# Kernel tuning notes

Hardware: AMD Instinct MI355X
Metric: run time of the kernel (lower is better)

Reference implementation:

```python
import jax, jax.numpy as jnp
import numpy as np

B, P, C, D, H = 32, 2048, 19, 512, 4
DH = D // H  # 128
EPS = 1e-5


def setup_inputs() -> dict:
    key = jax.random.key(0)
    ks = jax.random.split(key, 12)
    s = 0.02
    return {
        "x": jax.random.normal(ks[0], (B, P, D), jnp.float32),
        "channel_embeddings": jax.random.normal(ks[1], (C, D), jnp.float32),
        "Wq": jax.random.normal(ks[2], (D, D), jnp.float32) * s,
        "bq": jnp.zeros((D,), jnp.float32),
        "Wk": jax.random.normal(ks[3], (D, D), jnp.float32) * s,
        "bk": jnp.zeros((D,), jnp.float32),
        "Wv": jax.random.normal(ks[4], (D, D), jnp.float32) * s,
        "bv": jnp.zeros((D,), jnp.float32),
        "Wo": jax.random.normal(ks[5], (D, D), jnp.float32) * s,
        "bo": jnp.zeros((D,), jnp.float32),
        "gamma": jnp.ones((D,), jnp.float32),
        "beta": jnp.zeros((D,), jnp.float32),
    }


def reference(x, channel_embeddings, Wq, bq, Wk, bk, Wv, bv, Wo, bo, gamma, beta):
    # q: (B, P, H, DH)
    q = (x @ Wq.T + bq).reshape(B, P, H, DH)
    # K/V depend only on channel embeddings (same for every batch/patch in the
    # original; it merely materialized the broadcast). Compute once: (C, H, DH)
    k = (channel_embeddings @ Wk.T + bk).reshape(C, H, DH)
    v = (channel_embeddings @ Wv.T + bv).reshape(C, H, DH)
    # scores over channels: (B, P, C, H)
    scores = jnp.einsum("bphd,chd->bpch", q, k) / jnp.sqrt(jnp.float32(DH))
    weights = jax.nn.softmax(scores, axis=2)  # softmax over channel dim
    # weighted sum of channel values: (B, P, H, DH) -> (B, P, D)
    attended = jnp.einsum("bpch,chd->bphd", weights, v).reshape(B, P, D)
    out = attended @ Wo.T + bo  # dropout is identity in eval mode
    # residual + layernorm
    h = x + out
    mean = jnp.mean(h, axis=-1, keepdims=True)
    var = jnp.mean(jnp.square(h - mean), axis=-1, keepdims=True)
    return (h - mean) * jax.lax.rsqrt(var + EPS) * gamma + beta
```

## Files before the change

### kernel.cpp

```cpp
#include <hip/hip_runtime.h>
#include <hip/hip_bf16.h>

#define C_  19
#define D_  512
#define H_  4
#define DH_ 128
#define NROW 65536
#define CHP_ 96

typedef float f32x4 __attribute__((ext_vector_type(4)));
typedef short bf16x8 __attribute__((ext_vector_type(8)));

__device__ __forceinline__ unsigned short f2bf(float f) {
  union { __hip_bfloat16 h; unsigned short s; } u;
  u.h = __float2bfloat16(f);
  return u.s;
}
__device__ __forceinline__ float bf2f(unsigned short h) {
  return __uint_as_float(((unsigned int)h) << 16);
}
__device__ __forceinline__ bf16x8 ld_cvt8(const float* p) {
  f32x4 v0 = *(const f32x4*)p;
  f32x4 v1 = *(const f32x4*)(p + 4);
  bf16x8 a;
  a[0]=(short)f2bf(v0[0]); a[1]=(short)f2bf(v0[1]);
  a[2]=(short)f2bf(v0[2]); a[3]=(short)f2bf(v0[3]);
  a[4]=(short)f2bf(v1[0]); a[5]=(short)f2bf(v1[1]);
  a[6]=(short)f2bf(v1[2]); a[7]=(short)f2bf(v1[3]);
  return a;
}
__device__ __forceinline__ float dot4(f32x4 a, f32x4 b, float acc) {
  return fmaf(a[0],b[0], fmaf(a[1],b[1], fmaf(a[2],b[2], fmaf(a[3],b[3], acc))));
}

__global__ __launch_bounds__(512) void prep(
    const float* __restrict__ ce,
    const float* __restrict__ Wq, const float* __restrict__ bq,
    const float* __restrict__ Wk, const float* __restrict__ bk,
    const float* __restrict__ Wv, const float* __restrict__ bv,
    const float* __restrict__ Wo, const float* __restrict__ bo,
    unsigned short* __restrict__ Mtf, unsigned short* __restrict__ Utf,
    float* __restrict__ s0g)
{
  __shared__ __attribute__((aligned(16))) float KV[2][DH_];
  __shared__ float KVp[512];

  const int p = blockIdx.x;
  const int m = threadIdx.x;
  const int mt_off = (p>>4)*8192 + (m>>5)*512 + ((((m>>3)&3)<<4) + (p&15))*8 + (m&7);
  const int ut_off = ((m>>4)*3 + (p>>5))*512 + ((((p>>3)&3)<<4) + (m&15))*8 + (p&7);
  const int c = p >> 2, h = p & 3;

  if (c >= C_) {
    if (p < 80) { Mtf[mt_off] = 0; if (m == 0) s0g[p] = 0.f; }
    Utf[ut_off] = (p == 80) ? f2bf(bo[m]) : (unsigned short)0;
    return;
  }

  {
    const int which = m >> 8;
    const int dh    = (m >> 1) & 127;
    const int half  = m & 1;
    const float* w = (which ? Wv : Wk) + (size_t)(h*DH_ + dh)*D_ + half*256;
    const float* e = ce + (size_t)c*D_ + half*256;
    float a0 = 0.f, a1 = 0.f, a2 = 0.f, a3 = 0.f;
    #pragma unroll
    for (int d = 0; d < 256; d += 16) {
      a0 = dot4(*(const f32x4*)(w+d   ), *(const f32x4*)(e+d   ), a0);
      a1 = dot4(*(const f32x4*)(w+d+4 ), *(const f32x4*)(e+d+4 ), a1);
      a2 = dot4(*(const f32x4*)(w+d+8 ), *(const f32x4*)(e+d+8 ), a2);
      a3 = dot4(*(const f32x4*)(w+d+12), *(const f32x4*)(e+d+12), a3);
    }
    KVp[m] = (a0 + a1) + (a2 + a3);
  }
  __syncthreads();
  if (m < 256) {
    const int which = m >> 7, dh = m & 127;
    KV[which][dh] = KVp[2*m] + KVp[2*m+1] + (which ? bv : bk)[h*DH_ + dh];
  }
  __syncthreads();

  const float rs128 = 0.08838834764831843f;

  {
    float m0 = 0.f, m1 = 0.f, m2 = 0.f, m3 = 0.f;
    const float* wq = Wq + (size_t)(h*DH_)*D_ + m;
    #pragma unroll 8
    for (int dh = 0; dh < DH_; dh += 4) {
      m0 = fmaf(wq[(size_t)(dh  )*D_], KV[0][dh  ], m0);
      m1 = fmaf(wq[(size_t)(dh+1)*D_], KV[0][dh+1], m1);
      m2 = fmaf(wq[(size_t)(dh+2)*D_], KV[0][dh+2], m2);
      m3 = fmaf(wq[(size_t)(dh+3)*D_], KV[0][dh+3], m3);
    }
    Mtf[mt_off] = f2bf(((m0 + m1) + (m2 + m3)) * rs128);
  }

  {
    const float* wor = Wo + (size_t)m*D_ + h*DH_;
    float u0 = 0.f, u1 = 0.f, u2 = 0.f, u3 = 0.f;
    #pragma unroll
    for (int dh = 0; dh < DH_; dh += 16) {
      u0 = dot4(*(const f32x4*)(wor+dh   ), *(const f32x4*)(&KV[1][dh   ]), u0);
      u1 = dot4(*(const f32x4*)(wor+dh+4 ), *(const f32x4*)(&KV[1][dh+4 ]), u1);
      u2 = dot4(*(const f32x4*)(wor+dh+8 ), *(const f32x4*)(&KV[1][dh+8 ]), u2);
      u3 = dot4(*(const f32x4*)(wor+dh+12), *(const f32x4*)(&KV[1][dh+12]), u3);
    }
    Utf[ut_off] = f2bf((u0 + u1) + (u2 + u3));
  }

  if (m == 0) {
    float sa = 0.f;
    for (int dh = 0; dh < DH_; ++dh) sa = fmaf(bq[h*DH_+dh], KV[0][dh], sa);
    s0g[p] = sa * rs128;
  }
}

__global__ __launch_bounds__(256) void fused64(
    const float* __restrict__ x,
    const unsigned short* __restrict__ Mtf,
    const unsigned short* __restrict__ Utf,
    const float* __restrict__ s0g,
    const float* __restrict__ gamma, const float* __restrict__ beta,
    float* __restrict__ out)
{
  __shared__ __attribute__((aligned(16))) unsigned short Xbf[64*512];
  __shared__ __attribute__((aligned(16))) unsigned short WaL[64][104];
  __shared__ float rs_[64][2], rq_[64][2];

  const int t    = threadIdx.x;
  const int wave = t >> 6;
  const int lane = t & 63;
  const int lhi  = lane >> 4;
  const int llo  = lane & 15;
  const int row0 = blockIdx.x * 64;
  const int wrow = wave * 16;

  {
    #pragma unroll
    for (int j = 0; j < 16; ++j) {
      bf16x8 a = ld_cvt8(x + (size_t)(row0 + wrow + j)*D_ + lane*8);
      int byteoff = (wrow + j)*1024 + ((lane*16) ^ ((j & 7) << 4));
      *(bf16x8*)((char*)Xbf + byteoff) = a;
    }
  }
  asm volatile("s_waitcnt lgkmcnt(0)" ::: "memory");
  __builtin_amdgcn_sched_barrier(0);

  {
    const char* xb = (const char*)Xbf + (wrow + llo)*1024;
    const int swz = (llo & 7) << 4;
    f32x4 acc0 = (f32x4){0,0,0,0}, acc1 = acc0, acc2 = acc0, acc3 = acc0, acc4 = acc0;
    #pragma unroll
    for (int ks = 0; ks < 16; ++ks) {
      bf16x8 a = *(const bf16x8*)(xb + ((ks*64 + lhi*16) ^ swz));
      acc0 = __builtin_amdgcn_mfma_f32_16x16x32_bf16(a, *(const bf16x8*)(Mtf + 0*8192 + ks*512 + lane*8), acc0, 0, 0, 0);
      acc1 = __builtin_amdgcn_mfma_f32_16x16x32_bf16(a, *(const bf16x8*)(Mtf + 1*8192 + ks*512 + lane*8), acc1, 0, 0, 0);
      acc2 = __builtin_amdgcn_mfma_f32_16x16x32_bf16(a, *(const bf16x8*)(Mtf + 2*8192 + ks*512 + lane*8), acc2, 0, 0, 0);
      acc3 = __builtin_amdgcn_mfma_f32_16x16x32_bf16(a, *(const bf16x8*)(Mtf + 3*8192 + ks*512 + lane*8), acc3, 0, 0, 0);
      acc4 = __builtin_amdgcn_mfma_f32_16x16x32_bf16(a, *(const bf16x8*)(Mtf + 4*8192 + ks*512 + lane*8), acc4, 0, 0, 0);
    }
    const bool dead = (llo >= 12);
    float s0v0 = s0g[llo], s0v1 = s0g[16+llo], s0v2 = s0g[32+llo],
          s0v3 = s0g[48+llo], s0v4 = s0g[64+llo];
    #pragma unroll
    for (int r = 0; r < 4; ++r) {
      float v0 = acc0[r] + s0v0;
      float v1 = acc1[r] + s0v1;
      float v2 = acc2[r] + s0v2;
      float v3 = acc3[r] + s0v3;
      float v4 = dead ? -1e30f : (acc4[r] + s0v4);
      float mx = fmaxf(fmaxf(fmaxf(v0, v1), fmaxf(v2, v3)), v4);
      mx = fmaxf(mx, __shfl_xor(mx, 4, 64));
      mx = fmaxf(mx, __shfl_xor(mx, 8, 64));
      float e0 = __expf(v0 - mx), e1 = __expf(v1 - mx), e2 = __expf(v2 - mx),
            e3 = __expf(v3 - mx), e4 = dead ? 0.f : __expf(v4 - mx);
      float sm = e0 + e1 + e2 + e3 + e4;
      sm += __shfl_xor(sm, 4, 64);
      sm += __shfl_xor(sm, 8, 64);
      float inv = 1.f / sm;
      int lr = wrow + lhi*4 + r;
      WaL[lr][     llo] = f2bf(e0 * inv);
      WaL[lr][16 + llo] = f2bf(e1 * inv);
      WaL[lr][32 + llo] = f2bf(e2 * inv);
      WaL[lr][48 + llo] = f2bf(e3 * inv);
      WaL[lr][64 + llo] = f2bf(e4 * inv);
    }
    {
      int prow = wrow + lhi*4 + (llo & 3);
      int cj   = llo >> 2;
      WaL[prow][80 + cj*4 + 0] = (cj == 0) ? (unsigned short)0x3F80 : (unsigned short)0;
      WaL[prow][80 + cj*4 + 1] = 0;
      WaL[prow][80 + cj*4 + 2] = 0;
      WaL[prow][80 + cj*4 + 3] = 0;
    }
  }
  __syncthreads();

  const int rg = wave >> 1;
  const int cs = wave & 1;
  #pragma unroll
  for (int ha = 0; ha < 2; ++ha) {
    const int hrow = ha * 32;
    f32x4 oacc[16];
    #pragma unroll
    for (int i = 0; i < 16; ++i) oacc[i] = (f32x4){0.f,0.f,0.f,0.f};
    #pragma unroll
    for (int ks = 0; ks < 3; ++ks) {
      bf16x8 a = *(const bf16x8*)&WaL[hrow + rg*16 + llo][ks*32 + lhi*8];
      #pragma unroll
      for (int tile = 0; tile < 16; ++tile) {
        int ntile = cs*16 + tile;
        bf16x8 b = *(const bf16x8*)(Utf + (size_t)(ntile*3 + ks)*512 + lane*8);
        oacc[tile] = __builtin_amdgcn_mfma_f32_16x16x32_bf16(a, b, oacc[tile], 0, 0, 0);
      }
    }

    float s[4] = {0,0,0,0}, q[4] = {0,0,0,0};
    #pragma unroll
    for (int tile = 0; tile < 16; ++tile) {
      int n = cs*256 + tile*16 + llo;
      #pragma unroll
      for (int r = 0; r < 4; ++r) {
        int m = hrow + rg*16 + lhi*4 + r;
        float xres = bf2f(*(const unsigned short*)
            ((const char*)Xbf + m*1024 + ((n*2) ^ ((m & 7) << 4))));
        float val = oacc[tile][r] + xres;
        oacc[tile][r] = val;
        s[r] += val;
        q[r] = fmaf(val, val, q[r]);
      }
    }
    #pragma unroll
    for (int r = 0; r < 4; ++r) {
      #pragma unroll
      for (int off = 1; off < 16; off <<= 1) {
        s[r] += __shfl_xor(s[r], off, 64);
        q[r] += __shfl_xor(q[r], off, 64);
      }
    }
    if (llo == 0) {
      #pragma unroll
      for (int r = 0; r < 4; ++r) {
        rs_[hrow + rg*16 + lhi*4 + r][cs] = s[r];
        rq_[hrow + rg*16 + lhi*4 + r][cs] = q[r];
      }
    }
    __syncthreads();
    float mu_r[4], rstd_r[4];
    #pragma unroll
    for (int r = 0; r < 4; ++r) {
      int m = hrow + rg*16 + lhi*4 + r;
      float sum = rs_[m][0] + rs_[m][1];
      float sq  = rq_[m][0] + rq_[m][1];
      float mu  = sum * (1.f/(float)D_);
      float var = sq * (1.f/(float)D_) - mu*mu;
      mu_r[r]   = mu;
      rstd_r[r] = rsqrtf(var + 1e-5f);
    }
    #pragma unroll
    for (int tile = 0; tile < 16; ++tile) {
      int n = cs*256 + tile*16 + llo;
      float g = gamma[n], bt = beta[n];
      #pragma unroll
      for (int r = 0; r < 4; ++r) {
        int m = hrow + rg*16 + lhi*4 + r;
        out[(size_t)(row0 + m)*D_ + n] = (oacc[tile][r] - mu_r[r]) * rstd_r[r] * g + bt;
      }
    }
  }
}

extern "C" void kernel_launch(void* const* d_in, const int* in_sizes, int n_in,
                              void* d_out, int out_size, void* d_ws, size_t ws_size,
                              hipStream_t stream) {
  const float* x     = (const float*)d_in[0];
  const float* ce    = (const float*)d_in[1];
  const float* Wq    = (const float*)d_in[2];
  const float* bq    = (const float*)d_in[3];
  const float* Wk    = (const float*)d_in[4];
  const float* bk    = (const float*)d_in[5];
  const float* Wv    = (const float*)d_in[6];
  const float* bv    = (const float*)d_in[7];
  const float* Wo    = (const float*)d_in[8];
  const float* bo    = (const float*)d_in[9];
  const float* gamma = (const float*)d_in[10];
  const float* beta  = (const float*)d_in[11];
  float* out = (float*)d_out;

  char* ws = (char*)d_ws;
  unsigned short* Mtf = (unsigned short*)(ws);
  unsigned short* Utf = (unsigned short*)(ws + 81920);
  float* s0g          = (float*)(ws + 180224);

  prep<<<CHP_, 512, 0, stream>>>(ce, Wq, bq, Wk, bk, Wv, bv, Wo, bo,
                                 Mtf, Utf, s0g);
  fused64<<<NROW/64, 256, 0, stream>>>(x, Mtf, Utf, s0g, gamma, beta, out);
}
```

Before: 123.0 us.

## Split each 64-row tile across eight waves instead of four

The fused kernel now launches 512 threads per 64-row block, so each wave handles 8 rows in the first GEMM and a single 16-row half of the output GEMM and LayerNorm, instead of looping over two halves. The goal is more waves in flight per block and a shorter serial chain per wave, which helps latency hiding. In exchange, half of each first-stage MFMA's rows are redundant: lanes duplicate rows via llo&7 and only lhi<2 write. Launch bounds of 512 with a minimum of 4 blocks per unit also constrain register use.

After: 123.9 us. Within noise of the previous version (+0.7%).

```diff
diff --git a/kernel.cpp b/kernel.cpp
--- a/kernel.cpp
+++ b/kernel.cpp
@@ -115,7 +115,7 @@
   }
 }
 
-__global__ __launch_bounds__(256) void fused64(
+__global__ __launch_bounds__(512, 4) void fused64x8(
     const float* __restrict__ x,
     const unsigned short* __restrict__ Mtf,
     const unsigned short* __restrict__ Utf,
@@ -133,13 +133,13 @@
   const int lhi  = lane >> 4;
   const int llo  = lane & 15;
   const int row0 = blockIdx.x * 64;
-  const int wrow = wave * 16;
-
-  {
-    #pragma unroll
-    for (int j = 0; j < 16; ++j) {
+  const int wrow = wave * 8;
+
+  {
+    #pragma unroll
+    for (int j = 0; j < 8; ++j) {
       bf16x8 a = ld_cvt8(x + (size_t)(row0 + wrow + j)*D_ + lane*8);
-      int byteoff = (wrow + j)*1024 + ((lane*16) ^ ((j & 7) << 4));
+      int byteoff = (wrow + j)*1024 + ((lane*16) ^ (j << 4));
       *(bf16x8*)((char*)Xbf + byteoff) = a;
     }
   }
@@ -147,8 +147,9 @@
   __builtin_amdgcn_sched_barrier(0);
 
   {
-    const char* xb = (const char*)Xbf + (wrow + llo)*1024;
-    const int swz = (llo & 7) << 4;
+    const int arow = llo & 7;
+    const char* xb = (const char*)Xbf + (wrow + arow)*1024;
+    const int swz = arow << 4;
     f32x4 acc0 = (f32x4){0,0,0,0}, acc1 = acc0, acc2 = acc0, acc3 = acc0, acc4 = acc0;
     #pragma unroll
     for (int ks = 0; ks < 16; ++ks) {
@@ -178,16 +179,18 @@
       sm += __shfl_xor(sm, 4, 64);
       sm += __shfl_xor(sm, 8, 64);
       float inv = 1.f / sm;
-      int lr = wrow + lhi*4 + r;
-      WaL[lr][     llo] = f2bf(e0 * inv);
-      WaL[lr][16 + llo] = f2bf(e1 * inv);
-      WaL[lr][32 + llo] = f2bf(e2 * inv);
-      WaL[lr][48 + llo] = f2bf(e3 * inv);
-      WaL[lr][64 + llo] = f2bf(e4 * inv);
-    }
-    {
-      int prow = wrow + lhi*4 + (llo & 3);
-      int cj   = llo >> 2;
+      if (lhi < 2) {
+        int lr = wrow + lhi*4 + r;
+        WaL[lr][     llo] = f2bf(e0 * inv);
+        WaL[lr][16 + llo] = f2bf(e1 * inv);
+        WaL[lr][32 + llo] = f2bf(e2 * inv);
+        WaL[lr][48 + llo] = f2bf(e3 * inv);
+        WaL[lr][64 + llo] = f2bf(e4 * inv);
+      }
+    }
+    if (lane < 32) {
+      int prow = wrow + (lane & 7);
+      int cj   = (lane >> 3) & 3;
       WaL[prow][80 + cj*4 + 0] = (cj == 0) ? (unsigned short)0x3F80 : (unsigned short)0;
       WaL[prow][80 + cj*4 + 1] = 0;
       WaL[prow][80 + cj*4 + 2] = 0;
@@ -198,74 +201,70 @@
 
   const int rg = wave >> 1;
   const int cs = wave & 1;
-  #pragma unroll
-  for (int ha = 0; ha < 2; ++ha) {
-    const int hrow = ha * 32;
-    f32x4 oacc[16];
-    #pragma unroll
-    for (int i = 0; i < 16; ++i) oacc[i] = (f32x4){0.f,0.f,0.f,0.f};
-    #pragma unroll
-    for (int ks = 0; ks < 3; ++ks) {
-      bf16x8 a = *(const bf16x8*)&WaL[hrow + rg*16 + llo][ks*32 + lhi*8];
-      #pragma unroll
-      for (int tile = 0; tile < 16; ++tile) {
-        int ntile = cs*16 + tile;
-        bf16x8 b = *(const bf16x8*)(Utf + (size_t)(ntile*3 + ks)*512 + lane*8);
-        oacc[tile] = __builtin_amdgcn_mfma_f32_16x16x32_bf16(a, b, oacc[tile], 0, 0, 0);
-      }
-    }
-
-    float s[4] = {0,0,0,0}, q[4] = {0,0,0,0};
+  f32x4 oacc[16];
+  #pragma unroll
+  for (int i = 0; i < 16; ++i) oacc[i] = (f32x4){0.f,0.f,0.f,0.f};
+  #pragma unroll
+  for (int ks = 0; ks < 3; ++ks) {
+    bf16x8 a = *(const bf16x8*)&WaL[rg*16 + llo][ks*32 + lhi*8];
     #pragma unroll
     for (int tile = 0; tile < 16; ++tile) {
-      int n = cs*256 + tile*16 + llo;
-      #pragma unroll
-      for (int r = 0; r < 4; ++r) {
-        int m = hrow + rg*16 + lhi*4 + r;
-        float xres = bf2f(*(const unsigned short*)
-            ((const char*)Xbf + m*1024 + ((n*2) ^ ((m & 7) << 4))));
-        float val = oacc[tile][r] + xres;
-        oacc[tile][r] = val;
-        s[r] += val;
-        q[r] = fmaf(val, val, q[r]);
-      }
-    }
-    #pragma unroll
-    for (int r = 0; r < 4; ++r) {
-      #pragma unroll
-      for (int off = 1; off < 16; off <<= 1) {
-        s[r] += __shfl_xor(s[r], off, 64);
-        q[r] += __shfl_xor(q[r], off, 64);
-      }
-    }
-    if (llo == 0) {
-      #pragma unroll
-      for (int r = 0; r < 4; ++r) {
-        rs_[hrow + rg*16 + lhi*4 + r][cs] = s[r];
-        rq_[hrow + rg*16 + lhi*4 + r][cs] = q[r];
-      }
-    }
-    __syncthreads();
-    float mu_r[4], rstd_r[4];
-    #pragma unroll
-    for (int r = 0; r < 4; ++r) {
-      int m = hrow + rg*16 + lhi*4 + r;
-      float sum = rs_[m][0] + rs_[m][1];
-      float sq  = rq_[m][0] + rq_[m][1];
-      float mu  = sum * (1.f/(float)D_);
-      float var = sq * (1.f/(float)D_) - mu*mu;
-      mu_r[r]   = mu;
-      rstd_r[r] = rsqrtf(var + 1e-5f);
-    }
-    #pragma unroll
-    for (int tile = 0; tile < 16; ++tile) {
-      int n = cs*256 + tile*16 + llo;
-      float g = gamma[n], bt = beta[n];
-      #pragma unroll
-      for (int r = 0; r < 4; ++r) {
-        int m = hrow + rg*16 + lhi*4 + r;
-        out[(size_t)(row0 + m)*D_ + n] = (oacc[tile][r] - mu_r[r]) * rstd_r[r] * g + bt;
-      }
+      int ntile = cs*16 + tile;
+      bf16x8 b = *(const bf16x8*)(Utf + (size_t)(ntile*3 + ks)*512 + lane*8);
+      oacc[tile] = __builtin_amdgcn_mfma_f32_16x16x32_bf16(a, b, oacc[tile], 0, 0, 0);
+    }
+  }
+
+  float s[4] = {0,0,0,0}, q[4] = {0,0,0,0};
+  #pragma unroll
+  for (int tile = 0; tile < 16; ++tile) {
+    int n = cs*256 + tile*16 + llo;
+    #pragma unroll
+    for (int r = 0; r < 4; ++r) {
+      int m = rg*16 + lhi*4 + r;
+      float xres = bf2f(*(const unsigned short*)
+          ((const char*)Xbf + m*1024 + ((n*2) ^ ((m & 7) << 4))));
+      float val = oacc[tile][r] + xres;
+      oacc[tile][r] = val;
+      s[r] += val;
+      q[r] = fmaf(val, val, q[r]);
+    }
+  }
+  #pragma unroll
+  for (int r = 0; r < 4; ++r) {
+    #pragma unroll
+    for (int off = 1; off < 16; off <<= 1) {
+      s[r] += __shfl_xor(s[r], off, 64);
+      q[r] += __shfl_xor(q[r], off, 64);
+    }
+  }
+  if (llo == 0) {
+    #pragma unroll
+    for (int r = 0; r < 4; ++r) {
+      rs_[rg*16 + lhi*4 + r][cs] = s[r];
+      rq_[rg*16 + lhi*4 + r][cs] = q[r];
+    }
+  }
+  __syncthreads();
+  float mu_r[4], rstd_r[4];
+  #pragma unroll
+  for (int r = 0; r < 4; ++r) {
+    int m = rg*16 + lhi*4 + r;
+    float sum = rs_[m][0] + rs_[m][1];
+    float sq  = rq_[m][0] + rq_[m][1];
+    float mu  = sum * (1.f/(float)D_);
+    float var = sq * (1.f/(float)D_) - mu*mu;
+    mu_r[r]   = mu;
+    rstd_r[r] = rsqrtf(var + 1e-5f);
+  }
+  #pragma unroll
+  for (int tile = 0; tile < 16; ++tile) {
+    int n = cs*256 + tile*16 + llo;
+    float g = gamma[n], bt = beta[n];
+    #pragma unroll
+    for (int r = 0; r < 4; ++r) {
+      int m = rg*16 + lhi*4 + r;
+      out[(size_t)(row0 + m)*D_ + n] = (oacc[tile][r] - mu_r[r]) * rstd_r[r] * g + bt;
     }
   }
 }
@@ -294,5 +293,5 @@
 
   prep<<<CHP_, 512, 0, stream>>>(ce, Wq, bq, Wk, bk, Wv, bv, Wo, bo,
                                  Mtf, Utf, s0g);
-  fused64<<<NROW/64, 256, 0, stream>>>(x, Mtf, Utf, s0g, gamma, beta, out);
-}
+  fused64x8<<<NROW/64, 512, 0, stream>>>(x, Mtf, Utf, s0g, gamma, beta, out);
+}
```
